# Performance work log

Measured on AMD Instinct MI355X. Metric: run time of the kernel, lower is better.

The kernel has to match this reference:

```python
import jax, jax.numpy as jnp
import numpy as np

T, B, V, NG, H, MLP = 1024, 128, 128, 10, 1024, 128
F = V + NG  # feature_size = alphabet one-hot + genre one-hot


def setup_inputs() -> dict:
    key = jax.random.key(0)
    ks = jax.random.split(key, 14)
    s = 0.02
    inp = {
        "x": jax.random.normal(ks[0], (T, B, F), dtype=jnp.float32),
        # LSTMCell 1: input F -> hidden H (PyTorch layout: W_ih [4H, F], W_hh [4H, H])
        "W_ih1": jax.random.normal(ks[1], (4 * H, F), dtype=jnp.float32) * s,
        "b_ih1": jax.random.normal(ks[2], (4 * H,), dtype=jnp.float32) * s,
        "W_hh1": jax.random.normal(ks[3], (4 * H, H), dtype=jnp.float32) * s,
        "b_hh1": jax.random.normal(ks[4], (4 * H,), dtype=jnp.float32) * s,
        # LSTMCell 2: H -> H
        "W_ih2": jax.random.normal(ks[5], (4 * H, H), dtype=jnp.float32) * s,
        "b_ih2": jax.random.normal(ks[6], (4 * H,), dtype=jnp.float32) * s,
        "W_hh2": jax.random.normal(ks[7], (4 * H, H), dtype=jnp.float32) * s,
        "b_hh2": jax.random.normal(ks[8], (4 * H,), dtype=jnp.float32) * s,
        # MLP head: Linear(H,128) -> SELU -> Linear(128, V). Dropout(0.2) is identity in eval.
        "W1": jax.random.normal(ks[9], (MLP, H), dtype=jnp.float32) * s,
        "b1": jax.random.normal(ks[10], (MLP,), dtype=jnp.float32) * s,
        "W2": jax.random.normal(ks[11], (V, MLP), dtype=jnp.float32) * s,
        "b2": jax.random.normal(ks[12], (V,), dtype=jnp.float32) * s,
        "predict": 0,
    }
    return inp


def _lstm_cell(xt, h, c, W_ih, b_ih, W_hh, b_hh):
    # PyTorch LSTMCell gate order: input, forget, cell(g), output
    gates = xt @ W_ih.T + b_ih + h @ W_hh.T + b_hh  # [B, 4H]
    i, f, g, o = jnp.split(gates, 4, axis=-1)
    i, f, o = jax.nn.sigmoid(i), jax.nn.sigmoid(f), jax.nn.sigmoid(o)
    g = jnp.tanh(g)
    c_new = f * c + i * g
    h_new = o * jnp.tanh(c_new)
    return h_new, c_new


def reference(x, W_ih1, b_ih1, W_hh1, b_hh1, W_ih2, b_ih2, W_hh2, b_hh2,
              W1, b1, W2, b2, predict):
    n = x.shape[1]
    h0 = jnp.zeros((n, H), dtype=jnp.float32)
    init = (h0, h0, h0, h0)  # h_t, c_t, h2_t, c2_t

    def step(carry, xt):
        h, c, h2, c2 = carry
        h, c = _lstm_cell(xt, h, c, W_ih1, b_ih1, W_hh1, b_hh1)
        h2, c2 = _lstm_cell(h, h2, c2, W_ih2, b_ih2, W_hh2, b_hh2)
        out = jax.nn.selu(h2 @ W1.T + b1) @ W2.T + b2  # [B, V]
        return (h, c, h2, c2), out

    _, outputs = jax.lax.scan(step, init, x)  # [T, B, V]
    return outputs
```

## Files before the change

kernel.cpp:

```cpp
#include <hip/hip_runtime.h>
#include <cstdint>
#include <cstddef>

#define TT   1024
#define BB   128
#define FEAT 138
#define FPAD 160
#define HH   1024
#define VV   128
#define MM   128
#define K1   1184
#define K1P  1280
#define K2   2048
#define HCH  1024
#define H1N  131072
#define MIDN 16384
#define PKM1 1032
#define PKM2 136
#define OFF_RED 0
#define OFF_WM  32768
#define OFF_H   65792
#define OFF_M   67840
#define LDSZ    68864

typedef __bf16 bf16x8 __attribute__((ext_vector_type(8)));
typedef float  f32x4  __attribute__((ext_vector_type(4)));
typedef unsigned short u16;

__device__ __forceinline__ u16 f2bf(float f) {
  uint32_t u = __float_as_uint(f);
  u += 0x7fffu + ((u >> 16) & 1u);
  return (u16)(u >> 16);
}
__device__ __forceinline__ float sigm(float x) { return 1.0f / (1.0f + __expf(-x)); }
__device__ __forceinline__ float tanh_(float x) {
  float e = __expf(-2.0f * fabsf(x));
  float t = (1.0f - e) / (1.0f + e);
  return x < 0.0f ? -t : t;
}

__device__ __forceinline__ void stcc16(u16* p, uint4 v) {
  unsigned long long* p64 = (unsigned long long*)p;
  unsigned long long lo = ((unsigned long long)v.y << 32) | v.x;
  unsigned long long hi = ((unsigned long long)v.w << 32) | v.z;
  __hip_atomic_store(p64,     lo, __ATOMIC_RELAXED, __HIP_MEMORY_SCOPE_AGENT);
  __hip_atomic_store(p64 + 1, hi, __ATOMIC_RELAXED, __HIP_MEMORY_SCOPE_AGENT);
}

__global__ void conv_w1i(const float* __restrict__ Wih, const float* __restrict__ Whh,
                         const float* __restrict__ bi, const float* __restrict__ bh,
                         u16* __restrict__ dst, float* __restrict__ bsum) {
  int rp = blockIdx.x;
  int hc = rp >> 2, g = rp & 3;
  int sr = g * HH + hc;
  if (threadIdx.x == 0) bsum[rp] = bi[sr] + bh[sr];
  for (int k = threadIdx.x; k < K1P; k += 256) {
    float v = 0.0f;
    if (k < FPAD)    v = (k < FEAT) ? Wih[(size_t)sr * FEAT + k] : 0.0f;
    else if (k < K1) v = Whh[(size_t)sr * HH + (k - FPAD)];
    dst[(size_t)rp * K1P + k] = f2bf(v);
  }
}
__global__ void conv_w2i(const float* __restrict__ Wih, const float* __restrict__ Whh,
                         const float* __restrict__ bi, const float* __restrict__ bh,
                         u16* __restrict__ dst, float* __restrict__ bsum) {
  int rp = blockIdx.x;
  int hc = rp >> 2, g = rp & 3;
  int sr = g * HH + hc;
  if (threadIdx.x == 0) bsum[rp] = bi[sr] + bh[sr];
  for (int k = threadIdx.x; k < K2; k += 256) {
    float v = (k < HH) ? Wih[(size_t)sr * HH + k] : Whh[(size_t)sr * HH + (k - HH)];
    dst[(size_t)rp * K2 + k] = f2bf(v);
  }
}
__global__ void conv_mlpw(const float* __restrict__ W1, const float* __restrict__ W2,
                          u16* __restrict__ A, u16* __restrict__ Bm) {
  int i = blockIdx.x * 256 + threadIdx.x;
  if (i < MM * HH) A[i] = f2bf(W1[i]);
  else {
    int j = i - MM * HH;
    if (j < VV * MM) Bm[j] = f2bf(W2[j]);
  }
}
__global__ void conv_x(const float* __restrict__ x, u16* __restrict__ Xb) {
  int blk = blockIdx.x;
  int t = blk / 20, c = blk % 20;
  int b = threadIdx.x;
  if (b >= BB) return;
  const float* src = x + ((size_t)t * BB + b) * FEAT;
  u16 v[8];
#pragma unroll
  for (int e = 0; e < 8; ++e) {
    int col = c * 8 + e;
    v[e] = (col < FEAT) ? f2bf(src[col]) : (u16)0;
  }
  *(uint4*)(Xb + (((size_t)t * 20 + c) * BB + b) * 8) = *(uint4*)v;
}
__global__ void zero_ws(uint4* __restrict__ p, int n16) {
  int i = blockIdx.x * 256 + threadIdx.x;
  if (i < n16) p[i] = uint4{0, 0, 0, 0};
}


__device__ __forceinline__ void mfma_tile(const bf16x8& a0, const bf16x8& a1,
                                          const bf16x8 (&B)[4], f32x4 (&acc)[2][4]) {
#pragma unroll
  for (int n = 0; n < 4; ++n) {
    acc[0][n] = __builtin_amdgcn_mfma_f32_16x16x32_bf16(a0, B[n], acc[0][n], 0, 0, 0);
    acc[1][n] = __builtin_amdgcn_mfma_f32_16x16x32_bf16(a1, B[n], acc[1][n], 0, 0, 0);
  }
}
__device__ __forceinline__ void ld_tile(const u16* __restrict__ p, bf16x8 (&B)[4]) {
#pragma unroll
  for (int n = 0; n < 4; ++n) B[n] = *(const bf16x8*)(p + n * 128);
}
template<int NT, int OFS, int NA>
__device__ __forceinline__ void mac_ring(const bf16x8 (&A0)[NA], const bf16x8 (&A1)[NA],
                                         const u16* __restrict__ bp,
                                         f32x4 (&acc)[2][4]) {
  constexpr int D = NT < 4 ? NT : 4;
  bf16x8 Bq[D][4];
#pragma unroll
  for (int s = 0; s < D; ++s) ld_tile(bp + (size_t)s * 4096, Bq[s]);
#pragma unroll
  for (int s = 0; s < NT; ++s) {
    mfma_tile(A0[OFS + s], A1[OFS + s], Bq[s % D], acc);
    if (s + D < NT) ld_tile(bp + (size_t)(s + D) * 4096, Bq[s % D]);
  }
}

__device__ __forceinline__ void red_write(float* __restrict__ rg,
                                          const f32x4 (&acc)[2][4], int lane) {
#pragma unroll
  for (int mt = 0; mt < 2; ++mt)
#pragma unroll
    for (int n = 0; n < 4; ++n)
      *(f32x4*)(rg + (mt * 4 + n) * 256 + lane * 4) = acc[mt][n];
}
__device__ __forceinline__ void red_add(const float* __restrict__ rg,
                                        f32x4 (&acc)[2][4], int lane) {
#pragma unroll
  for (int mt = 0; mt < 2; ++mt)
#pragma unroll
    for (int n = 0; n < 4; ++n)
      acc[mt][n] += *(const f32x4*)(rg + (mt * 4 + n) * 256 + lane * 4);
}

__device__ __forceinline__ void lstm_tail(f32x4 (&acc)[2][4], const f32x4& bsv0,
                                          const f32x4& bsv1, float (&cst)[2][4],
                                          char* smem, int bh, int lane, int q, int l16,
                                          u16* __restrict__ houtChunk) {
  u16* st = (u16*)(smem + OFF_H) + bh * 512;
#pragma unroll
  for (int mt = 0; mt < 2; ++mt) {
    const f32x4 bsv = mt ? bsv1 : bsv0;
#pragma unroll
    for (int n = 0; n < 4; ++n) {
      float iv = sigm(acc[mt][n][0] + bsv[0]);
      float fv = sigm(acc[mt][n][1] + bsv[1]);
      float gv = tanh_(acc[mt][n][2] + bsv[2]);
      float ov = sigm(acc[mt][n][3] + bsv[3]);
      float c = fv * cst[mt][n] + iv * gv;
      cst[mt][n] = c;
      st[(n * 16 + l16) * 8 + mt * 4 + q] = f2bf(ov * tanh_(c));
    }
  }
  uint4 hv4 = *(uint4*)((u16*)(smem + OFF_H) + bh * 512 + lane * 8);
  stcc16(houtChunk + ((size_t)bh * 64 + lane) * 8, hv4);
}

template<bool ISL1>
__device__ __forceinline__ void wait_phase(const int* __restrict__ F, int p, int lane) {
  if (threadIdx.x < 64) {
    const int pa = p;
    const int pb = ISL1 ? p - 2 : p;
    for (;;) {
      int a = __hip_atomic_load(F + lane,       __ATOMIC_RELAXED, __HIP_MEMORY_SCOPE_AGENT);
      int b = __hip_atomic_load(F + 64 + lane,  __ATOMIC_RELAXED, __HIP_MEMORY_SCOPE_AGENT);
      int c = __hip_atomic_load(F + 128 + lane, __ATOMIC_RELAXED, __HIP_MEMORY_SCOPE_AGENT);
      int d = __hip_atomic_load(F + 192 + lane, __ATOMIC_RELAXED, __HIP_MEMORY_SCOPE_AGENT);
      if (__all(a >= pa && b >= pa && c >= pb && d >= pb)) break;
      __builtin_amdgcn_s_sleep(1);
    }
    __builtin_amdgcn_fence(__ATOMIC_ACQUIRE, "agent");
  }
  __syncthreads();
}
__device__ __forceinline__ void done_phase(int* __restrict__ slot, int p) {
  asm volatile("s_waitcnt vmcnt(0)" ::: "memory");
  __syncthreads();
  if (threadIdx.x == 0)
    __hip_atomic_store(slot, p + 1, __ATOMIC_RELAXED, __HIP_MEMORY_SCOPE_AGENT);
}

__device__ __forceinline__ void gbar(unsigned* __restrict__ bar, unsigned g) {
  asm volatile("s_waitcnt vmcnt(0)" ::: "memory");
  __syncthreads();
  if (threadIdx.x == 0) {
    unsigned v = __hip_atomic_fetch_add(&bar[(blockIdx.x & 7) * 16], 1u,
                                        __ATOMIC_RELAXED, __HIP_MEMORY_SCOPE_AGENT);
    if (v == 32u * g - 1u) {
      unsigned w = __hip_atomic_fetch_add(&bar[128], 1u,
                                          __ATOMIC_RELAXED, __HIP_MEMORY_SCOPE_AGENT);
      if (w == 8u * g - 1u)
        __hip_atomic_store(&bar[144], g, __ATOMIC_RELAXED, __HIP_MEMORY_SCOPE_AGENT);
    }
    __builtin_amdgcn_fence(__ATOMIC_ACQUIRE, "agent");
    while (__hip_atomic_load(&bar[144], __ATOMIC_RELAXED,
                             __HIP_MEMORY_SCOPE_AGENT) < g)
      __builtin_amdgcn_s_sleep(1);
  }
  __syncthreads();
}

template<int MODE>
__global__ __launch_bounds__(512, 2) void fused_lstm(
    const u16* __restrict__ W1i, const u16* __restrict__ W2i,
    const u16* __restrict__ W1m, const u16* __restrict__ W2m,
    const u16* __restrict__ Xb, u16* __restrict__ h1b, u16* __restrict__ h2b,
    u16* __restrict__ h2h, u16* __restrict__ midb,
    const float* __restrict__ bs1, const float* __restrict__ bs2,
    const float* __restrict__ bm1, const float* __restrict__ bm2,
    float* __restrict__ out, unsigned* __restrict__ bar)
{
  extern __shared__ char smem[];
  const int tid = threadIdx.x, bid = blockIdx.x;
  const int w = tid >> 6, lane = tid & 63, q = lane >> 4, l16 = lane & 15;
  const int kw = w & 3, bh = w >> 2;
  const bool isL1 = bid < 128;
  const int j = isL1 ? bid : bid - 128;
  float* red = (float*)(smem + OFF_RED);
  u16* Wm = (u16*)(smem + OFF_WM);
  int* flags = (int*)bar;
  const int SM = MODE ? 3 : 1;
  const int PEND = MODE ? (TT + 1) : (TT + 3);

  float cst[2][4] = {{0, 0, 0, 0}, {0, 0, 0, 0}};
  f32x4 bsv0 = {0, 0, 0, 0}, bsv1 = {0, 0, 0, 0};
  if (kw == 0) {
    const float* bs = isL1 ? bs1 : bs2;
    bsv0 = *(const f32x4*)(bs + (j * 8 + q) * 4);
    bsv1 = *(const f32x4*)(bs + (j * 8 + 4 + q) * 4);
  }

  if (isL1) {
    bf16x8 A1[2][10];
#pragma unroll
    for (int mt = 0; mt < 2; ++mt)
#pragma unroll
      for (int s = 0; s < 10; ++s)
        A1[mt][s] = *(const bf16x8*)(W1i + (size_t)(j * 32 + mt * 16 + l16) * K1P +
                                     (size_t)(kw * 10 + s) * 32 + q * 8);
    f32x4 bmv = {0, 0, 0, 0};
    if constexpr (MODE == 0) {
      if (j < 64) {
        int m0 = (j & 7) * 16;
        for (int i = tid; i < 16 * 128; i += 512) {
          int r = i >> 7, c8 = i & 127;
          *(uint4*)(Wm + r * PKM1 + c8 * 8) =
              *(const uint4*)(W1m + ((size_t)(m0 + r)) * HH + c8 * 8);
        }
      } else {
        int v0 = ((j - 64) & 7) * 16;
        for (int i = tid; i < 16 * 16; i += 512) {
          int r = i >> 4, c8 = i & 15;
          *(uint4*)(Wm + r * PKM2 + c8 * 8) =
              *(const uint4*)(W2m + ((size_t)(v0 + r)) * MM + c8 * 8);
        }
      }
      if (w == 3) {
        if (j < 64) bmv = *(const f32x4*)(bm1 + (j & 7) * 16 + q * 4);
        else        bmv = *(const f32x4*)(bm2 + ((j - 64) & 7) * 16 + q * 4);
      }
      __syncthreads();
    }

    for (int p = 0; p < PEND; ++p) {
      if constexpr (MODE == 1) wait_phase<true>(flags, p, lane);
      const bool act = p < TT;
      if (act) {
        const u16* h1p = h1b + (size_t)((p - 1) & SM) * H1N;
        f32x4 acc[2][4];
#pragma unroll
        for (int mt = 0; mt < 2; ++mt)
#pragma unroll
          for (int n = 0; n < 4; ++n) acc[mt][n] = (f32x4){0, 0, 0, 0};
        if (kw == 0) {
          const u16* bx = Xb + (size_t)p * 20480 +
                          ((size_t)q * 128 + bh * 64 + l16) * 8;
          mac_ring<5, 0, 10>(A1[0], A1[1], bx, acc);
          const u16* bp = h1p + ((size_t)q * 128 + bh * 64 + l16) * 8;
          mac_ring<5, 5, 10>(A1[0], A1[1], bp, acc);
        } else {
          const u16* bp = h1p + ((size_t)((kw * 10 - 5) * 4 + q) * 128 +
                                 bh * 64 + l16) * 8;
          if (kw == 3) mac_ring<7, 0, 10>(A1[0], A1[1], bp, acc);
          else         mac_ring<10, 0, 10>(A1[0], A1[1], bp, acc);
        }
        if (kw >= 2) red_write(red + (bh * 2 + kw - 2) * 2048, acc, lane);
        __syncthreads();
        if (kw < 2)  red_add(red + (bh * 2 + kw) * 2048, acc, lane);
        if (kw == 1) red_write(red + (bh * 2 + 1) * 2048, acc, lane);
        __syncthreads();
        if (kw == 0) {
          red_add(red + (bh * 2 + 1) * 2048, acc, lane);
          lstm_tail(acc, bsv0, bsv1, cst, smem, bh, lane, q, l16,
                    h1b + (size_t)(p & SM) * H1N + (size_t)j * HCH);
        }
      }
      if constexpr (MODE == 0) {
        if (w == 3) {
          if (j < 64) {
            if (p >= 2 && p <= TT + 1) {
              int jm = j & 7, jb = j >> 3;
              const u16* bsrc = h2b + (size_t)(p & 1) * H1N + q * HCH +
                                (jb * 16 + l16) * 8;
              const u16* am = Wm + l16 * PKM1 + q * 8;
              f32x4 acc = {0, 0, 0, 0};
#pragma unroll 4
              for (int s = 0; s < 32; ++s) {
                bf16x8 bf = *(const bf16x8*)(bsrc + (size_t)s * 4096);
                bf16x8 af = *(const bf16x8*)(am + s * 32);
                acc = __builtin_amdgcn_mfma_f32_16x16x32_bf16(af, bf, acc, 0, 0, 0);
              }
              const float SC = 1.0507009873554804934193349852946f;
              const float AL = 1.6732632423543772848170429916717f;
              u16* st16 = (u16*)(smem + OFF_M);
#pragma unroll
              for (int r = 0; r < 4; ++r) {
                float v = acc[r] + bmv[r];
                v = v > 0.0f ? SC * v : SC * AL * (__expf(v) - 1.0f);
                st16[l16 * 16 + q * 4 + r] = f2bf(v);
              }
              if (lane < 16) {
                uint4 v0 = *(uint4*)(st16 + lane * 16);
                uint4 v1 = *(uint4*)(st16 + lane * 16 + 8);
                u16* mc = midb + (size_t)(p & 1) * MIDN;
                stcc16(mc + (size_t)(2 * jm) * HCH + (jb * 16 + lane) * 8, v0);
                stcc16(mc + (size_t)(2 * jm + 1) * HCH + (jb * 16 + lane) * 8, v1);
              }
            }
          } else if (p >= 3) {
            int jj = j - 64, jv = jj & 7, jb = jj >> 3;
            const u16* bsrc = midb + (size_t)((p - 3) & 1) * MIDN + q * HCH +
                              (jb * 16 + l16) * 8;
            const u16* am = Wm + l16 * PKM2 + q * 8;
            f32x4 acc = {0, 0, 0, 0};
#pragma unroll
            for (int s = 0; s < 4; ++s) {
              bf16x8 bf = *(const bf16x8*)(bsrc + (size_t)s * 4096);
              bf16x8 af = *(const bf16x8*)(am + s * 32);
              acc = __builtin_amdgcn_mfma_f32_16x16x32_bf16(af, bf, acc, 0, 0, 0);
            }
            float* stf = (float*)(smem + OFF_M);
#pragma unroll
            for (int r = 0; r < 4; ++r) stf[l16 * 16 + q * 4 + r] = acc[r] + bmv[r];
            if (lane < 16) {
              float* orow = out + ((size_t)(p - 3) * BB + jb * 16 + lane) * VV + jv * 16;
              uint4* s4 = (uint4*)(stf + lane * 16);
              *(uint4*)(orow + 0)  = s4[0];
              *(uint4*)(orow + 4)  = s4[1];
              *(uint4*)(orow + 8)  = s4[2];
              *(uint4*)(orow + 12) = s4[3];
            }
          }
        }
        gbar(bar, (unsigned)p + 1u);
      } else {
        done_phase(flags + bid, p);
      }
    }
  } else {
    bf16x8 A2[2][16];
#pragma unroll
    for (int mt = 0; mt < 2; ++mt)
#pragma unroll
      for (int s = 0; s < 16; ++s)
        A2[mt][s] = *(const bf16x8*)(W2i + (size_t)(j * 32 + mt * 16 + l16) * K2 +
                                     (size_t)(kw * 16 + s) * 32 + q * 8);

    for (int p = 0; p < PEND; ++p) {
      if constexpr (MODE == 1) wait_phase<false>(flags, p, lane);
      const bool act = (p >= 1 && p <= TT);
      if (act) {
        const int t = p - 1;
        const u16* h1c = h1b + (size_t)(t & SM) * H1N;
        const u16* h2p = MODE ? (h2h + (size_t)t * H1N)
                              : (h2b + (size_t)((t - 1) & 1) * H1N);
        const u16* src = (kw < 2) ? h1c : h2p;
        const u16* bbase = src + ((size_t)((kw & 1) * 64 + q) * 128 +
                                  bh * 64 + l16) * 8;
        f32x4 acc[2][4];
#pragma unroll
        for (int mt = 0; mt < 2; ++mt)
#pragma unroll
          for (int n = 0; n < 4; ++n) acc[mt][n] = (f32x4){0, 0, 0, 0};
        mac_ring<16, 0, 16>(A2[0], A2[1], bbase, acc);

        if (kw >= 2) red_write(red + (bh * 2 + kw - 2) * 2048, acc, lane);
        __syncthreads();
        if (kw < 2)  red_add(red + (bh * 2 + kw) * 2048, acc, lane);
        if (kw == 1) red_write(red + (bh * 2 + 1) * 2048, acc, lane);
        __syncthreads();
        if (kw == 0) {
          red_add(red + (bh * 2 + 1) * 2048, acc, lane);
          u16* dst = MODE ? (h2h + (size_t)(t + 1) * H1N + (size_t)j * HCH)
                          : (h2b + (size_t)(t & 1) * H1N + (size_t)j * HCH);
          lstm_tail(acc, bsv0, bsv1, cst, smem, bh, lane, q, l16, dst);
        }
      }
      if constexpr (MODE == 0) gbar(bar, (unsigned)p + 1u);
      else                     done_phase(flags + bid, p);
    }
  }
}

__global__ __launch_bounds__(256) void mlp_head(
    const u16* __restrict__ W1m, const u16* __restrict__ W2m,
    const u16* __restrict__ h2h, const float* __restrict__ b1,
    const float* __restrict__ b2, float* __restrict__ out)
{
  __shared__ u16 midl[16 * 128 * 8];
  const int tid = threadIdx.x, t = blockIdx.x;
  const int wid = tid >> 6, lane = tid & 63, q = lane >> 4, l16 = lane & 15;
  const u16* h2t = h2h + (size_t)(t + 1) * H1N;
  const int mbase = wid * 32;

  f32x4 acc[2][8];
#pragma unroll
  for (int a = 0; a < 2; ++a)
#pragma unroll
    for (int n = 0; n < 8; ++n) acc[a][n] = (f32x4){0, 0, 0, 0};
#pragma unroll 2
  for (int kc = 0; kc < 32; ++kc) {
    bf16x8 a0 = *(const bf16x8*)(W1m + (size_t)(mbase + l16) * HH + kc * 32 + q * 8);
    bf16x8 a1 = *(const bf16x8*)(W1m + (size_t)(mbase + 16 + l16) * HH + kc * 32 + q * 8);
    const u16* bp = h2t + (size_t)(kc * 4 + q) * 1024 + l16 * 8;
#pragma unroll
    for (int n = 0; n < 8; ++n) {
      bf16x8 bf = *(const bf16x8*)(bp + n * 128);
      acc[0][n] = __builtin_amdgcn_mfma_f32_16x16x32_bf16(a0, bf, acc[0][n], 0, 0, 0);
      acc[1][n] = __builtin_amdgcn_mfma_f32_16x16x32_bf16(a1, bf, acc[1][n], 0, 0, 0);
    }
  }
  const float SC = 1.0507009873554804934193349852946f;
  const float AL = 1.6732632423543772848170429916717f;
  f32x4 bm0 = *(const f32x4*)(b1 + mbase + q * 4);
  f32x4 bm1v = *(const f32x4*)(b1 + mbase + 16 + q * 4);
#pragma unroll
  for (int mt = 0; mt < 2; ++mt) {
    const f32x4 bm = mt ? bm1v : bm0;
    const int m0 = mbase + mt * 16 + q * 4;
#pragma unroll
    for (int n = 0; n < 8; ++n) {
      const int b = n * 16 + l16;
#pragma unroll
      for (int r = 0; r < 4; ++r) {
        float v = acc[mt][n][r] + bm[r];
        v = v > 0.0f ? SC * v : SC * AL * (__expf(v) - 1.0f);
        int mm = m0 + r;
        midl[(mm >> 3) * 1024 + b * 8 + (mm & 7)] = f2bf(v);
      }
    }
  }
  __syncthreads();
  f32x4 acc2[2][8];
#pragma unroll
  for (int a = 0; a < 2; ++a)
#pragma unroll
    for (int n = 0; n < 8; ++n) acc2[a][n] = (f32x4){0, 0, 0, 0};
#pragma unroll
  for (int kc = 0; kc < 4; ++kc) {
    bf16x8 a0 = *(const bf16x8*)(W2m + (size_t)(mbase + l16) * MM + kc * 32 + q * 8);
    bf16x8 a1 = *(const bf16x8*)(W2m + (size_t)(mbase + 16 + l16) * MM + kc * 32 + q * 8);
    const u16* bp = midl + (kc * 4 + q) * 1024 + l16 * 8;
#pragma unroll
    for (int n = 0; n < 8; ++n) {
      bf16x8 bf = *(const bf16x8*)(bp + n * 128);
      acc2[0][n] = __builtin_amdgcn_mfma_f32_16x16x32_bf16(a0, bf, acc2[0][n], 0, 0, 0);
      acc2[1][n] = __builtin_amdgcn_mfma_f32_16x16x32_bf16(a1, bf, acc2[1][n], 0, 0, 0);
    }
  }
  f32x4 c0 = *(const f32x4*)(b2 + mbase + q * 4);
  f32x4 c1 = *(const f32x4*)(b2 + mbase + 16 + q * 4);
  float* ot = out + (size_t)t * BB * VV;
#pragma unroll
  for (int mt = 0; mt < 2; ++mt)
#pragma unroll
    for (int n = 0; n < 8; ++n) {
      f32x4 v = acc2[mt][n] + (mt ? c1 : c0);
      *(f32x4*)(ot + (size_t)(n * 16 + l16) * VV + mbase + mt * 16 + q * 4) = v;
    }
}

extern "C" void kernel_launch(void* const* d_in, const int* in_sizes, int n_in,
                              void* d_out, int out_size, void* d_ws, size_t ws_size,
                              hipStream_t stream)
{
  const float* x    = (const float*)d_in[0];
  const float* Wih1 = (const float*)d_in[1];
  const float* bih1 = (const float*)d_in[2];
  const float* Whh1 = (const float*)d_in[3];
  const float* bhh1 = (const float*)d_in[4];
  const float* Wih2 = (const float*)d_in[5];
  const float* bih2 = (const float*)d_in[6];
  const float* Whh2 = (const float*)d_in[7];
  const float* bhh2 = (const float*)d_in[8];
  const float* W1   = (const float*)d_in[9];
  const float* b1   = (const float*)d_in[10];
  const float* W2   = (const float*)d_in[11];
  const float* b2   = (const float*)d_in[12];
  float* out = (float*)d_out;
  (void)in_sizes; (void)n_in; (void)out_size;

  char* ws = (char*)d_ws;
  size_t off = 0;
  auto alloc = [&](size_t n) { char* p = ws + off; off += (n + 255) & ~(size_t)255; return p; };
  u16* W1i   = (u16*)alloc((size_t)4096 * K1P * 2);
  u16* W2i   = (u16*)alloc((size_t)4096 * K2 * 2);
  u16* W1m   = (u16*)alloc((size_t)MM * HH * 2);
  u16* W2m   = (u16*)alloc((size_t)VV * MM * 2);
  u16* Xb    = (u16*)alloc((size_t)TT * 20 * BB * 8 * 2);
  float* bs1 = (float*)alloc(4096 * 4);
  float* bs2 = (float*)alloc(4096 * 4);
  u16* h1b   = (u16*)alloc(4 * (size_t)H1N * 2 + 32768);
  u16* h2b   = (u16*)alloc(2 * (size_t)H1N * 2);
  u16* midb  = (u16*)alloc(2 * (size_t)MIDN * 2);
  unsigned* bar = (unsigned*)alloc(4096);
  size_t off_base = off;
  u16* h2h   = (u16*)alloc((size_t)(TT + 1) * H1N * 2);
  const bool postMLP = ws_size >= off;
  if (ws_size < off_base) return;

  conv_w1i<<<4096, 256, 0, stream>>>(Wih1, Whh1, bih1, bhh1, W1i, bs1);
  conv_w2i<<<4096, 256, 0, stream>>>(Wih2, Whh2, bih2, bhh2, W2i, bs2);
  conv_mlpw<<<576, 256, 0, stream>>>(W1, W2, W1m, W2m);
  conv_x<<<TT * 20, 128, 0, stream>>>(x, Xb);
  {
    int n16 = (int)((4 * (size_t)H1N * 2 + 32768 + 2 * (size_t)H1N * 2 +
                     2 * (size_t)MIDN * 2 + 4096) / 16);
    zero_ws<<<(n16 + 255) / 256, 256, 0, stream>>>((uint4*)h1b, n16);
  }
  if (postMLP) {
    zero_ws<<<(H1N * 2 / 16 + 255) / 256, 256, 0, stream>>>((uint4*)h2h, H1N * 2 / 16);
  }

  using KFn = void (*)(const u16*, const u16*, const u16*, const u16*, const u16*,
                       u16*, u16*, u16*, u16*, const float*, const float*,
                       const float*, const float*, float*, unsigned*);
  KFn fp = postMLP ? (KFn)fused_lstm<1> : (KFn)fused_lstm<0>;
  (void)hipFuncSetAttribute((const void*)fp,
                            hipFuncAttributeMaxDynamicSharedMemorySize, LDSZ);
  void* args[] = { (void*)&W1i, (void*)&W2i, (void*)&W1m, (void*)&W2m,
                   (void*)&Xb, (void*)&h1b, (void*)&h2b, (void*)&h2h, (void*)&midb,
                   (void*)&bs1, (void*)&bs2, (void*)&b1, (void*)&b2,
                   (void*)&out, (void*)&bar };
  hipError_t err = hipLaunchCooperativeKernel((const void*)fp,
                                              dim3(256), dim3(512), args, LDSZ, stream);
  if (err != hipSuccess) {
    if (postMLP)
      fused_lstm<1><<<dim3(256), dim3(512), LDSZ, stream>>>(
          W1i, W2i, W1m, W2m, Xb, h1b, h2b, h2h, midb, bs1, bs2, b1, b2, out, bar);
    else
      fused_lstm<0><<<dim3(256), dim3(512), LDSZ, stream>>>(
          W1i, W2i, W1m, W2m, Xb, h1b, h2b, h2h, midb, bs1, bs2, b1, b2, out, bar);
  }
  if (postMLP) {
    mlp_head<<<dim3(TT), dim3(256), 0, stream>>>(W1m, W2m, h2h, b1, b2, out);
  }
}
```

Baseline: 14.74 ms.

## Store full layer-1 hidden history to loosen layer coupling and drop acquire fence

Adds a mode that writes every layer-1 hidden state into a full time-indexed history buffer instead of a 4-slot ring. Because no slot is reused, layer 1 can run up to six steps ahead of layer 2 instead of two, which reduces stalls in the flag-based cross-block wait. The agent-scope acquire fence after the spin wait is also skipped in this mode. The cost is a workspace buffer of roughly 270MB and a risk of reading stale data without the fence.

```diff
diff --git a/kernel.cpp b/kernel.cpp
--- a/kernel.cpp
+++ b/kernel.cpp
@@ -169,11 +169,11 @@
   stcc16(houtChunk + ((size_t)bh * 64 + lane) * 8, hv4);
 }
 
-template<bool ISL1>
+template<int MODE, bool ISL1>
 __device__ __forceinline__ void wait_phase(const int* __restrict__ F, int p, int lane) {
   if (threadIdx.x < 64) {
     const int pa = p;
-    const int pb = ISL1 ? p - 2 : p;
+    const int pb = ISL1 ? (MODE == 2 ? p - 6 : p - 2) : p;
     for (;;) {
       int a = __hip_atomic_load(F + lane,       __ATOMIC_RELAXED, __HIP_MEMORY_SCOPE_AGENT);
       int b = __hip_atomic_load(F + 64 + lane,  __ATOMIC_RELAXED, __HIP_MEMORY_SCOPE_AGENT);
@@ -182,7 +182,8 @@
       if (__all(a >= pa && b >= pa && c >= pb && d >= pb)) break;
       __builtin_amdgcn_s_sleep(1);
     }
-    __builtin_amdgcn_fence(__ATOMIC_ACQUIRE, "agent");
+    if constexpr (MODE == 1)
+      __builtin_amdgcn_fence(__ATOMIC_ACQUIRE, "agent");
   }
   __syncthreads();
 }
@@ -217,8 +218,8 @@
 __global__ __launch_bounds__(512, 2) void fused_lstm(
     const u16* __restrict__ W1i, const u16* __restrict__ W2i,
     const u16* __restrict__ W1m, const u16* __restrict__ W2m,
-    const u16* __restrict__ Xb, u16* __restrict__ h1b, u16* __restrict__ h2b,
-    u16* __restrict__ h2h, u16* __restrict__ midb,
+    const u16* __restrict__ Xb, u16* __restrict__ h1b, u16* __restrict__ h1h,
+    u16* __restrict__ h2b, u16* __restrict__ h2h, u16* __restrict__ midb,
     const float* __restrict__ bs1, const float* __restrict__ bs2,
     const float* __restrict__ bm1, const float* __restrict__ bm2,
     float* __restrict__ out, unsigned* __restrict__ bar)
@@ -232,8 +233,6 @@
   float* red = (float*)(smem + OFF_RED);
   u16* Wm = (u16*)(smem + OFF_WM);
   int* flags = (int*)bar;
-  const int SM = MODE ? 3 : 1;
-  const int PEND = MODE ? (TT + 1) : (TT + 3);
 
   float cst[2][4] = {{0, 0, 0, 0}, {0, 0, 0, 0}};
   f32x4 bsv0 = {0, 0, 0, 0}, bsv1 = {0, 0, 0, 0};
@@ -275,11 +274,13 @@
       __syncthreads();
     }
 
-    for (int p = 0; p < PEND; ++p) {
-      if constexpr (MODE == 1) wait_phase<true>(flags, p, lane);
+    const int PL = (MODE == 0) ? TT + 3 : (MODE == 1 ? TT + 1 : TT);
+    for (int p = 0; p < PL; ++p) {
+      if constexpr (MODE >= 1) wait_phase<MODE, true>(flags, p, lane);
       const bool act = p < TT;
       if (act) {
-        const u16* h1p = h1b + (size_t)((p - 1) & SM) * H1N;
+        const u16* h1p = (MODE == 2) ? (h1h + (size_t)p * H1N)
+                                     : (h1b + (size_t)((p - 1) & (MODE ? 3 : 1)) * H1N);
         f32x4 acc[2][4];
 #pragma unroll
         for (int mt = 0; mt < 2; ++mt)
@@ -304,8 +305,10 @@
         __syncthreads();
         if (kw == 0) {
           red_add(red + (bh * 2 + 1) * 2048, acc, lane);
-          lstm_tail(acc, bsv0, bsv1, cst, smem, bh, lane, q, l16,
-                    h1b + (size_t)(p & SM) * H1N + (size_t)j * HCH);
+          u16* hdst = (MODE == 2) ? (h1h + (size_t)(p + 1) * H1N + (size_t)j * HCH)
+                                  : (h1b + (size_t)(p & (MODE ? 3 : 1)) * H1N +
+                                     (size_t)j * HCH);
+          lstm_tail(acc, bsv0, bsv1, cst, smem, bh, lane, q, l16, hdst);
         }
       }
       if constexpr (MODE == 0) {
@@ -379,12 +382,14 @@
         A2[mt][s] = *(const bf16x8*)(W2i + (size_t)(j * 32 + mt * 16 + l16) * K2 +
                                      (size_t)(kw * 16 + s) * 32 + q * 8);
 
-    for (int p = 0; p < PEND; ++p) {
-      if constexpr (MODE == 1) wait_phase<false>(flags, p, lane);
+    const int PL = (MODE == 0) ? TT + 3 : TT + 1;
+    for (int p = 0; p < PL; ++p) {
+      if constexpr (MODE >= 1) wait_phase<MODE, false>(flags, p, lane);
       const bool act = (p >= 1 && p <= TT);
       if (act) {
         const int t = p - 1;
-        const u16* h1c = h1b + (size_t)(t & SM) * H1N;
+        const u16* h1c = (MODE == 2) ? (h1h + (size_t)(t + 1) * H1N)
+                                     : (h1b + (size_t)(t & (MODE ? 3 : 1)) * H1N);
         const u16* h2p = MODE ? (h2h + (size_t)t * H1N)
                               : (h2b + (size_t)((t - 1) & 1) * H1N);
         const u16* src = (kw < 2) ? h1c : h2p;
@@ -529,7 +534,10 @@
   unsigned* bar = (unsigned*)alloc(4096);
   size_t off_base = off;
   u16* h2h   = (u16*)alloc((size_t)(TT + 1) * H1N * 2);
-  const bool postMLP = ws_size >= off;
+  size_t off_h2h = off;
+  u16* h1h   = (u16*)alloc((size_t)(TT + 1) * H1N * 2);
+  size_t off_full = off;
+  int mode = (ws_size >= off_full) ? 2 : (ws_size >= off_h2h ? 1 : 0);
   if (ws_size < off_base) return;
 
   conv_w1i<<<4096, 256, 0, stream>>>(Wih1, Whh1, bih1, bhh1, W1i, bs1);
@@ -541,31 +549,38 @@
                      2 * (size_t)MIDN * 2 + 4096) / 16);
     zero_ws<<<(n16 + 255) / 256, 256, 0, stream>>>((uint4*)h1b, n16);
   }
-  if (postMLP) {
+  if (mode >= 1) {
     zero_ws<<<(H1N * 2 / 16 + 255) / 256, 256, 0, stream>>>((uint4*)h2h, H1N * 2 / 16);
   }
+  if (mode == 2) {
+    zero_ws<<<(H1N * 2 / 16 + 255) / 256, 256, 0, stream>>>((uint4*)h1h, H1N * 2 / 16);
+  }
 
   using KFn = void (*)(const u16*, const u16*, const u16*, const u16*, const u16*,
-                       u16*, u16*, u16*, u16*, const float*, const float*,
+                       u16*, u16*, u16*, u16*, u16*, const float*, const float*,
                        const float*, const float*, float*, unsigned*);
-  KFn fp = postMLP ? (KFn)fused_lstm<1> : (KFn)fused_lstm<0>;
+  KFn fp = (mode == 2) ? (KFn)fused_lstm<2>
+         : (mode == 1) ? (KFn)fused_lstm<1> : (KFn)fused_lstm<0>;
   (void)hipFuncSetAttribute((const void*)fp,
                             hipFuncAttributeMaxDynamicSharedMemorySize, LDSZ);
   void* args[] = { (void*)&W1i, (void*)&W2i, (void*)&W1m, (void*)&W2m,
-                   (void*)&Xb, (void*)&h1b, (void*)&h2b, (void*)&h2h, (void*)&midb,
-                   (void*)&bs1, (void*)&bs2, (void*)&b1, (void*)&b2,
+                   (void*)&Xb, (void*)&h1b, (void*)&h1h, (void*)&h2b, (void*)&h2h,
+                   (void*)&midb, (void*)&bs1, (void*)&bs2, (void*)&b1, (void*)&b2,
                    (void*)&out, (void*)&bar };
   hipError_t err = hipLaunchCooperativeKernel((const void*)fp,
                                               dim3(256), dim3(512), args, LDSZ, stream);
   if (err != hipSuccess) {
-    if (postMLP)
+    if (mode == 2)
+      fused_lstm<2><<<dim3(256), dim3(512), LDSZ, stream>>>(
+          W1i, W2i, W1m, W2m, Xb, h1b, h1h, h2b, h2h, midb, bs1, bs2, b1, b2, out, bar);
+    else if (mode == 1)
       fused_lstm<1><<<dim3(256), dim3(512), LDSZ, stream>>>(
-          W1i, W2i, W1m, W2m, Xb, h1b, h2b, h2h, midb, bs1, bs2, b1, b2, out, bar);
+          W1i, W2i, W1m, W2m, Xb, h1b, h1h, h2b, h2h, midb, bs1, bs2, b1, b2, out, bar);
     else
       fused_lstm<0><<<dim3(256), dim3(512), LDSZ, stream>>>(
-          W1i, W2i, W1m, W2m, Xb, h1b, h2b, h2h, midb, bs1, bs2, b1, b2, out, bar);
-  }
-  if (postMLP) {
+          W1i, W2i, W1m, W2m, Xb, h1b, h1h, h2b, h2h, midb, bs1, bs2, b1, b2, out, bar);
+  }
+  if (mode >= 1) {
     mlp_head<<<dim3(TT), dim3(256), 0, stream>>>(W1m, W2m, h2h, b1, b2, out);
   }
 }
```

New measurement: 14.91 ms. No clear change (+1.2%).

## Deepen layer-1 h ring to 16 slots and let layer 1 run further ahead

Applied to the files above, without the earlier changes.

Grows the layer-1 hidden-state ring buffer from 4 to 16 slots and relaxes the flag wait so layer-1 blocks may run up to 6 steps ahead of layer-2 consumers instead of 2. The acquire fence also moves before the spin loop, so each block has more slack to absorb timing jitter between the two pipelined layers. The cost is a larger workspace to zero and wider skew. Placing the fence before the polling may weaken acquire ordering for the data being waited on.

```diff
diff --git a/kernel.cpp b/kernel.cpp
--- a/kernel.cpp
+++ b/kernel.cpp
@@ -169,11 +169,13 @@
   stcc16(houtChunk + ((size_t)bh * 64 + lane) * 8, hv4);
 }
 
-template<bool ISL1>
+template<int MODE, bool ISL1>
 __device__ __forceinline__ void wait_phase(const int* __restrict__ F, int p, int lane) {
   if (threadIdx.x < 64) {
+    if ((MODE == 1) || ((p & 3) == 0))
+      __builtin_amdgcn_fence(__ATOMIC_ACQUIRE, "agent");
     const int pa = p;
-    const int pb = ISL1 ? p - 2 : p;
+    const int pb = ISL1 ? (MODE == 3 ? p - 6 : p - 2) : p;
     for (;;) {
       int a = __hip_atomic_load(F + lane,       __ATOMIC_RELAXED, __HIP_MEMORY_SCOPE_AGENT);
       int b = __hip_atomic_load(F + 64 + lane,  __ATOMIC_RELAXED, __HIP_MEMORY_SCOPE_AGENT);
@@ -182,7 +184,6 @@
       if (__all(a >= pa && b >= pa && c >= pb && d >= pb)) break;
       __builtin_amdgcn_s_sleep(1);
     }
-    __builtin_amdgcn_fence(__ATOMIC_ACQUIRE, "agent");
   }
   __syncthreads();
 }
@@ -232,8 +233,7 @@
   float* red = (float*)(smem + OFF_RED);
   u16* Wm = (u16*)(smem + OFF_WM);
   int* flags = (int*)bar;
-  const int SM = MODE ? 3 : 1;
-  const int PEND = MODE ? (TT + 1) : (TT + 3);
+  const int SM = (MODE == 3) ? 15 : 1;
 
   float cst[2][4] = {{0, 0, 0, 0}, {0, 0, 0, 0}};
   f32x4 bsv0 = {0, 0, 0, 0}, bsv1 = {0, 0, 0, 0};
@@ -275,8 +275,9 @@
       __syncthreads();
     }
 
-    for (int p = 0; p < PEND; ++p) {
-      if constexpr (MODE == 1) wait_phase<true>(flags, p, lane);
+    const int PL = (MODE == 0) ? TT + 3 : TT;
+    for (int p = 0; p < PL; ++p) {
+      if constexpr (MODE != 0) wait_phase<MODE, true>(flags, p, lane);
       const bool act = p < TT;
       if (act) {
         const u16* h1p = h1b + (size_t)((p - 1) & SM) * H1N;
@@ -379,14 +380,15 @@
         A2[mt][s] = *(const bf16x8*)(W2i + (size_t)(j * 32 + mt * 16 + l16) * K2 +
                                      (size_t)(kw * 16 + s) * 32 + q * 8);
 
-    for (int p = 0; p < PEND; ++p) {
-      if constexpr (MODE == 1) wait_phase<false>(flags, p, lane);
+    const int PL = (MODE == 0) ? TT + 3 : TT + 1;
+    for (int p = 0; p < PL; ++p) {
+      if constexpr (MODE != 0) wait_phase<MODE, false>(flags, p, lane);
       const bool act = (p >= 1 && p <= TT);
       if (act) {
         const int t = p - 1;
         const u16* h1c = h1b + (size_t)(t & SM) * H1N;
-        const u16* h2p = MODE ? (h2h + (size_t)t * H1N)
-                              : (h2b + (size_t)((t - 1) & 1) * H1N);
+        const u16* h2p = (MODE == 3) ? (h2h + (size_t)t * H1N)
+                                     : (h2b + (size_t)((t - 1) & 1) * H1N);
         const u16* src = (kw < 2) ? h1c : h2p;
         const u16* bbase = src + ((size_t)((kw & 1) * 64 + q) * 128 +
                                   bh * 64 + l16) * 8;
@@ -404,8 +406,8 @@
         __syncthreads();
         if (kw == 0) {
           red_add(red + (bh * 2 + 1) * 2048, acc, lane);
-          u16* dst = MODE ? (h2h + (size_t)(t + 1) * H1N + (size_t)j * HCH)
-                          : (h2b + (size_t)(t & 1) * H1N + (size_t)j * HCH);
+          u16* dst = (MODE == 3) ? (h2h + (size_t)(t + 1) * H1N + (size_t)j * HCH)
+                                 : (h2b + (size_t)(t & 1) * H1N + (size_t)j * HCH);
           lstm_tail(acc, bsv0, bsv1, cst, smem, bh, lane, q, l16, dst);
         }
       }
@@ -523,13 +525,14 @@
   u16* Xb    = (u16*)alloc((size_t)TT * 20 * BB * 8 * 2);
   float* bs1 = (float*)alloc(4096 * 4);
   float* bs2 = (float*)alloc(4096 * 4);
-  u16* h1b   = (u16*)alloc(4 * (size_t)H1N * 2 + 32768);
+  u16* h1b   = (u16*)alloc(16 * (size_t)H1N * 2 + 32768);
   u16* h2b   = (u16*)alloc(2 * (size_t)H1N * 2);
   u16* midb  = (u16*)alloc(2 * (size_t)MIDN * 2);
   unsigned* bar = (unsigned*)alloc(4096);
   size_t off_base = off;
   u16* h2h   = (u16*)alloc((size_t)(TT + 1) * H1N * 2);
-  const bool postMLP = ws_size >= off;
+  size_t off_h2h = off;
+  int mode = (ws_size >= off_h2h) ? 3 : 0;
   if (ws_size < off_base) return;
 
   conv_w1i<<<4096, 256, 0, stream>>>(Wih1, Whh1, bih1, bhh1, W1i, bs1);
@@ -537,18 +540,18 @@
   conv_mlpw<<<576, 256, 0, stream>>>(W1, W2, W1m, W2m);
   conv_x<<<TT * 20, 128, 0, stream>>>(x, Xb);
   {
-    int n16 = (int)((4 * (size_t)H1N * 2 + 32768 + 2 * (size_t)H1N * 2 +
+    int n16 = (int)((16 * (size_t)H1N * 2 + 32768 + 2 * (size_t)H1N * 2 +
                      2 * (size_t)MIDN * 2 + 4096) / 16);
     zero_ws<<<(n16 + 255) / 256, 256, 0, stream>>>((uint4*)h1b, n16);
   }
-  if (postMLP) {
+  if (mode == 3) {
     zero_ws<<<(H1N * 2 / 16 + 255) / 256, 256, 0, stream>>>((uint4*)h2h, H1N * 2 / 16);
   }
 
   using KFn = void (*)(const u16*, const u16*, const u16*, const u16*, const u16*,
                        u16*, u16*, u16*, u16*, const float*, const float*,
                        const float*, const float*, float*, unsigned*);
-  KFn fp = postMLP ? (KFn)fused_lstm<1> : (KFn)fused_lstm<0>;
+  KFn fp = (mode == 3) ? (KFn)fused_lstm<3> : (KFn)fused_lstm<0>;
   (void)hipFuncSetAttribute((const void*)fp,
                             hipFuncAttributeMaxDynamicSharedMemorySize, LDSZ);
   void* args[] = { (void*)&W1i, (void*)&W2i, (void*)&W1m, (void*)&W2m,
@@ -558,14 +561,14 @@
   hipError_t err = hipLaunchCooperativeKernel((const void*)fp,
                                               dim3(256), dim3(512), args, LDSZ, stream);
   if (err != hipSuccess) {
-    if (postMLP)
-      fused_lstm<1><<<dim3(256), dim3(512), LDSZ, stream>>>(
+    if (mode == 3)
+      fused_lstm<3><<<dim3(256), dim3(512), LDSZ, stream>>>(
           W1i, W2i, W1m, W2m, Xb, h1b, h2b, h2h, midb, bs1, bs2, b1, b2, out, bar);
     else
       fused_lstm<0><<<dim3(256), dim3(512), LDSZ, stream>>>(
           W1i, W2i, W1m, W2m, Xb, h1b, h2b, h2h, midb, bs1, bs2, b1, b2, out, bar);
   }
-  if (postMLP) {
+  if (mode == 3) {
     mlp_head<<<dim3(TT), dim3(256), 0, stream>>>(W1m, W2m, h2h, b1, b2, out);
   }
 }
```

Measured after the change: 14.88 ms. About the same (+1.0%).
